# Kernel optimization log

Hardware: AMD Instinct MI355X
Metric: run time of the kernel (lower is better)

## Reference

```python
import jax, jax.numpy as jnp
import numpy as np

B, L, E, H = 2, 2048, 1024, 16
D = E // H  # head dim = 64


def setup_inputs() -> dict:
    key = jax.random.key(0)
    ks = jax.random.split(key, 10)
    s = 0.02
    return {
        "xt": jax.random.normal(ks[0], (B, L, E), jnp.float32),
        "xs": jax.random.normal(ks[1], (B, L, E), jnp.float32),
        "Wt": jax.random.normal(ks[2], (E, 3 * E), jnp.float32) * s,  # t_attn weight (x @ Wt)
        "bt": jnp.zeros((3 * E,), jnp.float32),
        "Ws": jax.random.normal(ks[3], (E, 2 * E), jnp.float32) * s,  # s_attn weight
        "bs": jnp.zeros((2 * E,), jnp.float32),
        "Wc": jax.random.normal(ks[4], (E, E), jnp.float32) * s,      # c_proj weight
        "bc": jnp.zeros((E,), jnp.float32),
        "lam_ts": jnp.ones((1,), jnp.float32),
        "lam_st": jnp.ones((1,), jnp.float32),
        "lam_ss": jnp.ones((1,), jnp.float32),
    }


def _heads(x):
    # (B, L, E) -> (B, H, L, D)
    return x.reshape(B, L, H, D).transpose(0, 2, 1, 3)


def reference(xt, xs, Wt, bt, Ws, bs, Wc, bc, lam_ts, lam_st, lam_ss):
    qt, kt, vt = jnp.split(xt @ Wt + bt, 3, axis=2)
    qs, ks = jnp.split(xs @ Ws + bs, 2, axis=2)
    qt, kt, vt, qs, ks = map(_heads, (qt, kt, vt, qs, ks))

    # 4-way disentangled scores; fuse the 4 matmuls into 2 by combining keys:
    # qt@kt^T + lam_ts*qt@ks^T = qt @ (kt + lam_ts*ks)^T
    # lam_st*qs@kt^T + lam_ss*qs@ks^T = qs @ (lam_st*kt + lam_ss*ks)^T
    k1 = kt + lam_ts[0] * ks
    k2 = lam_st[0] * kt + lam_ss[0] * ks
    att = (jnp.einsum('bhqd,bhkd->bhqk', qt, k1)
           + jnp.einsum('bhqd,bhkd->bhqk', qs, k2)) * (1.0 / np.sqrt(D))
    att = jax.nn.softmax(att, axis=-1)
    y = jnp.einsum('bhqk,bhkd->bhqd', att, vt)  # (B, H, L, D)
    y = y.transpose(0, 2, 1, 3).reshape(B, L, E)
    return y @ Wc + bc
```

## Files before the change

kernel.cpp:

```cpp
#include <hip/hip_runtime.h>
#include <math.h>

#define LQ 2048
#define EQ 1024
#define M_ROWS 4096
#define BH 32

typedef _Float16 f16x8 __attribute__((ext_vector_type(8)));
typedef _Float16 f16x4 __attribute__((ext_vector_type(4)));
typedef _Float16 f16x2 __attribute__((ext_vector_type(2)));
typedef float f32x4 __attribute__((ext_vector_type(4)));
typedef float f32x16 __attribute__((ext_vector_type(16)));

#define QSCALE 0.1803368801111204f

__device__ __forceinline__ void async_ld16(const _Float16* g, _Float16* l) {
  __builtin_amdgcn_global_load_lds(
      (const __attribute__((address_space(1))) unsigned int*)g,
      (__attribute__((address_space(3))) unsigned int*)l, 16, 0, 0);
}

__global__ __launch_bounds__(256) void prep(
    const float* __restrict__ xt, const float* __restrict__ xs,
    const float* __restrict__ Wt, const float* __restrict__ Ws,
    const float* __restrict__ Wc,
    _Float16* __restrict__ xt16, _Float16* __restrict__ xs16,
    _Float16* __restrict__ WtT, _Float16* __restrict__ WsT,
    _Float16* __restrict__ WcT) {
  int gb = blockIdx.x;
  if (gb < 4096) {
    int i = gb * 256 + threadIdx.x;
    const float* s; _Float16* d; size_t off;
    if (i < 524288) { s = xt; d = xt16; off = (size_t)i * 8; }
    else            { s = xs; d = xs16; off = (size_t)(i - 524288) * 8; }
    float4 a = *(const float4*)&s[off];
    float4 b = *(const float4*)&s[off + 4];
    f16x8 h;
    h[0] = (_Float16)a.x; h[1] = (_Float16)a.y; h[2] = (_Float16)a.z; h[3] = (_Float16)a.w;
    h[4] = (_Float16)b.x; h[5] = (_Float16)b.y; h[6] = (_Float16)b.z; h[7] = (_Float16)b.w;
    *(f16x8*)&d[off] = h;
  } else {
    __shared__ float T[32][65];
    int tb = gb - 4096;
    int c0 = (tb % 96) * 64;
    int k0 = (tb / 96) * 32;
    const float* W; _Float16* D; int Nw, cl;
    if (c0 < 3072)      { W = Wt; D = WtT; Nw = 3072; cl = c0; }
    else if (c0 < 5120) { W = Ws; D = WsT; Nw = 2048; cl = c0 - 3072; }
    else                { W = Wc; D = WcT; Nw = 1024; cl = c0 - 5120; }
    const int tid = threadIdx.x;
#pragma unroll
    for (int p = 0; p < 4; ++p) {
      int idx = tid + p * 256;
      int row = idx >> 5;
      int c2 = (idx & 31) * 2;
      float2 v = *(const float2*)&W[(size_t)(k0 + row) * Nw + cl + c2];
      T[row][c2] = v.x;
      T[row][c2 + 1] = v.y;
    }
    __syncthreads();
#pragma unroll
    for (int p = 0; p < 4; ++p) {
      int idx = tid + p * 256;
      int col = idx >> 4;
      int k2 = (idx & 15) * 2;
      f16x2 h2;
      h2[0] = (_Float16)T[k2][col];
      h2[1] = (_Float16)T[k2 + 1][col];
      *(f16x2*)&D[(size_t)(cl + col) * 1024 + k0 + k2] = h2;
    }
  }
}

__global__ __launch_bounds__(256, 3) void proj_gemm(
    const _Float16* __restrict__ xt16, const _Float16* __restrict__ xs16,
    const _Float16* __restrict__ WtT, const _Float16* __restrict__ WsT,
    const float* __restrict__ bt, const float* __restrict__ bs,
    _Float16* __restrict__ q16, _Float16* __restrict__ k16,
    _Float16* __restrict__ v16) {
  __shared__ _Float16 Al[128 * 64];
  __shared__ _Float16 Bl[128 * 64];

  const int tid = threadIdx.x;
  const int w = tid >> 6;
  const int lane = tid & 63;
  const int quad = lane >> 4;
  const int l15 = lane & 15;
  const int wm = w >> 1, wn = w & 1;
  const int by = blockIdx.y;
  const int n0 = blockIdx.x * 128;

  const _Float16* Ab;
  const _Float16* Bb;
  const float* bias;
  int m0, bsel = 0, branch;
  if (by < 32) {
    branch = 0; Ab = xt16; Bb = WtT; bias = bt; m0 = by * 128;
  } else if (by < 48) {
    branch = 1;
    int by2 = by - 32;
    bsel = by2 >> 3;
    m0 = (by2 & 7) * 128;
    Ab = WtT + (size_t)2048 * 1024;
    Bb = xt16 + (size_t)bsel * 2048 * 1024;
    bias = bt;
  } else {
    branch = 2; Ab = xs16; Bb = WsT; bias = bs; m0 = (by - 48) * 128;
  }

  const int srow = lane >> 3;
  const int sch = lane & 7;

  f32x4 acc[4][4];
#pragma unroll
  for (int mb = 0; mb < 4; ++mb)
#pragma unroll
    for (int nb = 0; nb < 4; ++nb) acc[mb][nb] = (f32x4){0.f, 0.f, 0.f, 0.f};

  for (int kt = 0; kt < 1024; kt += 64) {
    __syncthreads();
#pragma unroll
    for (int a = 0; a < 4; ++a) {
      int row = w * 32 + a * 8 + srow;
      int sc = sch ^ (row & 7);
      async_ld16(&Ab[(size_t)(m0 + row) * 1024 + kt + sc * 8], &Al[(w * 32 + a * 8) * 64]);
      async_ld16(&Bb[(size_t)(n0 + row) * 1024 + kt + sc * 8], &Bl[(w * 32 + a * 8) * 64]);
    }
    __syncthreads();

#pragma unroll
    for (int g = 0; g < 2; ++g) {
      f16x8 af[4], bf[4];
#pragma unroll
      for (int mb = 0; mb < 4; ++mb) {
        int row = wm * 64 + mb * 16 + l15;
        int pc = ((g * 4 + quad) ^ (row & 7)) * 8;
        af[mb] = *(const f16x8*)&Al[row * 64 + pc];
      }
#pragma unroll
      for (int nb = 0; nb < 4; ++nb) {
        int row = wn * 64 + nb * 16 + l15;
        int pc = ((g * 4 + quad) ^ (row & 7)) * 8;
        bf[nb] = *(const f16x8*)&Bl[row * 64 + pc];
      }
#pragma unroll
      for (int mb = 0; mb < 4; ++mb)
#pragma unroll
        for (int nb = 0; nb < 4; ++nb)
          acc[mb][nb] = __builtin_amdgcn_mfma_f32_16x16x32_f16(af[mb], bf[nb], acc[mb][nb], 0, 0, 0);
    }
  }

#pragma unroll
  for (int mb = 0; mb < 4; ++mb)
#pragma unroll
    for (int nb = 0; nb < 4; ++nb)
#pragma unroll
      for (int r = 0; r < 4; ++r) {
        int row = m0 + wm * 64 + mb * 16 + quad * 4 + r;
        int col = n0 + wn * 64 + nb * 16 + l15;
        if (branch == 1) {
          float val = acc[mb][nb][r] + bias[2048 + row];
          v16[(size_t)(bsel * 1024 + row) * 2048 + col] = (_Float16)val;
        } else {
          float val = acc[mb][nb][r] + bias[col];
          int bb = row >> 11, ll = row & 2047;
          int which = col >> 10, e = col & 1023;
          int hh = e >> 6, dd = e & 63;
          size_t rowhd = (size_t)(bb * 16 + hh) * 2048 + ll;
          int off = (branch == 0) ? 0 : 64;
          if (which == 0) q16[rowhd * 128 + off + dd] = (_Float16)val;
          else            k16[rowhd * 128 + off + dd] = (_Float16)val;
        }
      }
}

__global__ __launch_bounds__(256, 3) void cproj_gemm(
    const _Float16* __restrict__ A, const _Float16* __restrict__ Bm,
    const float* __restrict__ bias, float* __restrict__ outf) {
  __shared__ _Float16 Al0[128 * 32];
  __shared__ _Float16 Bl0[64 * 32];
  __shared__ _Float16 Al1[128 * 32];
  __shared__ _Float16 Bl1[64 * 32];

  const int tid = threadIdx.x;
  const int w = tid >> 6;
  const int lane = tid & 63;
  const int quad = lane >> 4;
  const int l15 = lane & 15;
  const int wm = w >> 1, wn = w & 1;
  const int m0 = blockIdx.y * 128;
  const int n0 = blockIdx.x * 64;

  const int srow = lane >> 2;
  const int schunk = ((lane & 3) ^ ((lane >> 3) & 3)) * 8;

  f32x4 acc[4][2];
#pragma unroll
  for (int mb = 0; mb < 4; ++mb)
#pragma unroll
    for (int nb = 0; nb < 2; ++nb) acc[mb][nb] = (f32x4){0.f, 0.f, 0.f, 0.f};

  const int key = (l15 >> 1) & 3;

  auto dma = [&](int kt, _Float16* Al, _Float16* Bl) {
#pragma unroll
    for (int i = 0; i < 2; ++i) {
      int rt = w * 32 + i * 16;
      async_ld16(&A[(size_t)(m0 + rt + srow) * 1024 + kt + schunk], &Al[rt * 32]);
    }
    int rtb = w * 16;
    async_ld16(&Bm[(size_t)(n0 + rtb + srow) * 1024 + kt + schunk], &Bl[rtb * 32]);
  };

  auto comp = [&](const _Float16* Al, const _Float16* Bl) {
    f16x8 af[4], bf[2];
    const int pc = (quad ^ key) * 8;
#pragma unroll
    for (int mb = 0; mb < 4; ++mb)
      af[mb] = *(const f16x8*)&Al[(wm * 64 + mb * 16 + l15) * 32 + pc];
#pragma unroll
    for (int nb = 0; nb < 2; ++nb)
      bf[nb] = *(const f16x8*)&Bl[(wn * 32 + nb * 16 + l15) * 32 + pc];
#pragma unroll
    for (int mb = 0; mb < 4; ++mb)
#pragma unroll
      for (int nb = 0; nb < 2; ++nb)
        acc[mb][nb] = __builtin_amdgcn_mfma_f32_16x16x32_f16(af[mb], bf[nb], acc[mb][nb], 0, 0, 0);
  };

  dma(0, Al0, Bl0);
  for (int kt = 0; kt < 1024; kt += 64) {
    __syncthreads();
    dma(kt + 32, Al1, Bl1);
    comp(Al0, Bl0);
    __syncthreads();
    if (kt + 64 < 1024) dma(kt + 64, Al0, Bl0);
    comp(Al1, Bl1);
  }

#pragma unroll
  for (int mb = 0; mb < 4; ++mb)
#pragma unroll
    for (int nb = 0; nb < 2; ++nb)
#pragma unroll
      for (int r = 0; r < 4; ++r) {
        int row = m0 + wm * 64 + mb * 16 + quad * 4 + r;
        int col = n0 + wn * 32 + nb * 16 + l15;
        outf[(size_t)row * 1024 + col] = acc[mb][nb][r] + bias[col];
      }
}

__global__ __launch_bounds__(256, 2) void flash_attn_mfma(
    const _Float16* __restrict__ qcat, const _Float16* __restrict__ kcat,
    const _Float16* __restrict__ vT, _Float16* __restrict__ y,
    const float* __restrict__ lam_ts, const float* __restrict__ lam_st,
    const float* __restrict__ lam_ss) {
  const int bh = blockIdx.y;
  const int qt0 = blockIdx.x * 128;
  const int b = bh >> 4, h = bh & 15;
  const _Float16* Qg = qcat + (size_t)bh * LQ * 128;
  const _Float16* Kg = kcat + (size_t)bh * LQ * 128;
  const _Float16* Vg = vT + (size_t)bh * 64 * LQ;

  __shared__ _Float16 Ksh0[64 * 128];
  __shared__ _Float16 Ksh1[64 * 128];
  __shared__ _Float16 Vsh0[64 * 64];
  __shared__ _Float16 Vsh1[64 * 64];

  const int tid = threadIdx.x;
  const int w = tid >> 6;
  const int lane = tid & 63;
  const int half = lane >> 5;
  const int l31 = lane & 31;

  const float lts = lam_ts[0], lst = lam_st[0], lss = lam_ss[0];

  f16x8 qf[8];
#pragma unroll
  for (int db = 0; db < 4; ++db) {
    const _Float16* qp = &Qg[(size_t)(qt0 + w * 32 + l31) * 128 + db * 16 + half * 8];
    f16x8 a = *(const f16x8*)qp;
    f16x8 bq = *(const f16x8*)(qp + 64);
#pragma unroll
    for (int e = 0; e < 8; ++e) {
      float fa = (float)a[e], fb = (float)bq[e];
      qf[db][e]     = (_Float16)(QSCALE * (fa + lst * fb));
      qf[db + 4][e] = (_Float16)(QSCALE * (lts * fa + lss * fb));
    }
  }

  float m_i = -INFINITY;
  float l_i = 0.f;
  f32x16 O[2];
#pragma unroll
  for (int nt = 0; nt < 2; ++nt)
#pragma unroll
    for (int r = 0; r < 16; ++r) O[nt][r] = 0.f;

  auto dma = [&](int t, _Float16* Kd, _Float16* Vd) {
#pragma unroll
    for (int a = 0; a < 4; ++a) {
      int row = w * 16 + a * 4 + (lane >> 4);
      int sc = (lane & 15) ^ (row & 7);
      async_ld16(&Kg[(size_t)(t + row) * 128 + sc * 8], &Kd[(w * 16 + a * 4) * 128]);
    }
#pragma unroll
    for (int a = 0; a < 2; ++a) {
      int row = w * 16 + a * 8 + (lane >> 3);
      int sc = (lane & 7) ^ (row & 7);
      async_ld16(&Vg[(size_t)row * LQ + t + sc * 8], &Vd[(w * 16 + a * 8) * 64]);
    }
  };

  auto compute = [&](const _Float16* Ks, const _Float16* Vs) {
    f32x16 S[2];
#pragma unroll
    for (int kb = 0; kb < 2; ++kb)
#pragma unroll
      for (int r = 0; r < 16; ++r) S[kb][r] = 0.f;
#pragma unroll
    for (int db = 0; db < 8; ++db) {
      const int pc = ((db * 2 + half) ^ (lane & 7)) * 8;
      f16x8 af[2];
#pragma unroll
      for (int kb = 0; kb < 2; ++kb)
        af[kb] = *(const f16x8*)&Ks[(kb * 32 + l31) * 128 + pc];
#pragma unroll
      for (int kb = 0; kb < 2; ++kb)
        S[kb] = __builtin_amdgcn_mfma_f32_32x32x16_f16(af[kb], qf[db], S[kb], 0, 0, 0);
    }

    float mx = -INFINITY;
#pragma unroll
    for (int kb = 0; kb < 2; ++kb)
#pragma unroll
      for (int r = 0; r < 16; ++r) mx = fmaxf(mx, S[kb][r]);
    mx = fmaxf(mx, __shfl_xor(mx, 32));
    float m_new = fmaxf(m_i, mx);
    float alpha = __builtin_amdgcn_exp2f(m_i - m_new);
    float s = 0.f;
#pragma unroll
    for (int kb = 0; kb < 2; ++kb)
#pragma unroll
      for (int r = 0; r < 16; ++r) {
        float p = __builtin_amdgcn_exp2f(S[kb][r] - m_new);
        S[kb][r] = p;
        s += p;
      }
    s += __shfl_xor(s, 32);
    l_i = l_i * alpha + s;
    m_i = m_new;

#pragma unroll
    for (int nt = 0; nt < 2; ++nt)
#pragma unroll
      for (int r = 0; r < 16; ++r) O[nt][r] *= alpha;

    unsigned pu[2][8];
#pragma unroll
    for (int kb = 0; kb < 2; ++kb)
#pragma unroll
      for (int i = 0; i < 8; ++i) {
        f16x2 t2;
        t2[0] = (_Float16)S[kb][2 * i];
        t2[1] = (_Float16)S[kb][2 * i + 1];
        pu[kb][i] = __builtin_bit_cast(unsigned, t2);
      }

#pragma unroll
    for (int kb = 0; kb < 2; ++kb)
#pragma unroll
      for (int c = 0; c < 2; ++c) {
        unsigned ulo0 = pu[kb][4 * c + 0], ulo1 = pu[kb][4 * c + 1];
        unsigned uhi0 = pu[kb][4 * c + 2], uhi1 = pu[kb][4 * c + 3];
        unsigned rlo0 = (unsigned)__shfl_xor((int)ulo0, 32);
        unsigned rlo1 = (unsigned)__shfl_xor((int)ulo1, 32);
        unsigned rhi0 = (unsigned)__shfl_xor((int)uhi0, 32);
        unsigned rhi1 = (unsigned)__shfl_xor((int)uhi1, 32);
        union { unsigned u[4]; f16x8 v; } pb;
        pb.u[0] = half ? rhi0 : ulo0;
        pb.u[1] = half ? rhi1 : ulo1;
        pb.u[2] = half ? uhi0 : rlo0;
        pb.u[3] = half ? uhi1 : rlo1;
        int kb2 = kb * 2 + c;
        f16x8 av[2];
#pragma unroll
        for (int nt = 0; nt < 2; ++nt) {
          int dim = nt * 32 + l31;
          int pc = ((kb2 * 2 + half) ^ (dim & 7)) * 8;
          av[nt] = *(const f16x8*)&Vs[dim * 64 + pc];
        }
#pragma unroll
        for (int nt = 0; nt < 2; ++nt)
          O[nt] = __builtin_amdgcn_mfma_f32_32x32x16_f16(av[nt], pb.v, O[nt], 0, 0, 0);
      }
  };

  dma(0, Ksh0, Vsh0);
  for (int t = 0; t < LQ; t += 128) {
    __syncthreads();
    dma(t + 64, Ksh1, Vsh1);
    compute(Ksh0, Vsh0);
    __syncthreads();
    if (t + 128 < LQ) dma(t + 128, Ksh0, Vsh0);
    compute(Ksh1, Vsh1);
  }

  float inv = 1.f / l_i;
  int qrow = qt0 + w * 32 + l31;
#pragma unroll
  for (int nt = 0; nt < 2; ++nt)
#pragma unroll
    for (int rg = 0; rg < 4; ++rg) {
      f16x4 o4;
#pragma unroll
      for (int i = 0; i < 4; ++i) o4[i] = (_Float16)(O[nt][rg * 4 + i] * inv);
      int dim = nt * 32 + rg * 8 + half * 4;
      *(f16x4*)&y[((size_t)b * LQ + qrow) * EQ + h * 64 + dim] = o4;
    }
}

extern "C" void kernel_launch(void* const* d_in, const int* in_sizes, int n_in,
                              void* d_out, int out_size, void* d_ws, size_t ws_size,
                              hipStream_t stream) {
  const float* xt = (const float*)d_in[0];
  const float* xs = (const float*)d_in[1];
  const float* Wt = (const float*)d_in[2];
  const float* bt = (const float*)d_in[3];
  const float* Ws = (const float*)d_in[4];
  const float* bs = (const float*)d_in[5];
  const float* Wc = (const float*)d_in[6];
  const float* bc = (const float*)d_in[7];
  const float* lam_ts = (const float*)d_in[8];
  const float* lam_st = (const float*)d_in[9];
  const float* lam_ss = (const float*)d_in[10];
  float* out = (float*)d_out;

  _Float16* w16 = (_Float16*)d_ws;
  _Float16* xt16 = w16;
  _Float16* xs16 = xt16 + 4194304;
  _Float16* WtT  = xs16 + 4194304;
  _Float16* WsT  = WtT + 3145728;
  _Float16* WcT  = WsT + 2097152;
  _Float16* qcat = WcT + 1048576;
  _Float16* kcat = qcat + 8388608;
  _Float16* vbufT = kcat + 8388608;
  _Float16* ybuf = vbufT + 4194304;

  prep<<<7168, 256, 0, stream>>>(xt, xs, Wt, Ws, Wc, xt16, xs16, WtT, WsT, WcT);
  proj_gemm<<<dim3(16, 80), 256, 0, stream>>>(
      xt16, xs16, WtT, WsT, bt, bs, qcat, kcat, vbufT);
  flash_attn_mfma<<<dim3(16, 32), 256, 0, stream>>>(
      qcat, kcat, vbufT, ybuf, lam_ts, lam_st, lam_ss);
  cproj_gemm<<<dim3(16, 32), 256, 0, stream>>>(ybuf, WcT, bc, out);
}
```

Baseline: 263.7 us.

## Split attention KV range in two and merge partial softmax results

The flash attention kernel now processes half of the key sequence per block, using a third grid dimension. It writes unnormalized fp32 partial outputs plus row max and sum, and a new merge kernel combines them into the fp16 attention output. Launch bounds are raised to 3 blocks per CU. The goal is more parallel blocks and better CU utilization, at the cost of extra global traffic for the partials, another launch, and possible register pressure.

```diff
diff --git a/kernel.cpp b/kernel.cpp
--- a/kernel.cpp
+++ b/kernel.cpp
@@ -251,14 +251,16 @@
       }
 }
 
-__global__ __launch_bounds__(256, 2) void flash_attn_mfma(
+__global__ __launch_bounds__(256, 3) void flash_attn_mfma(
     const _Float16* __restrict__ qcat, const _Float16* __restrict__ kcat,
-    const _Float16* __restrict__ vT, _Float16* __restrict__ y,
+    const _Float16* __restrict__ vT,
+    float* __restrict__ Opart, float* __restrict__ MLpart,
     const float* __restrict__ lam_ts, const float* __restrict__ lam_st,
     const float* __restrict__ lam_ss) {
   const int bh = blockIdx.y;
   const int qt0 = blockIdx.x * 128;
-  const int b = bh >> 4, h = bh & 15;
+  const int split = blockIdx.z;
+  const int t0 = split * 1024;
   const _Float16* Qg = qcat + (size_t)bh * LQ * 128;
   const _Float16* Kg = kcat + (size_t)bh * LQ * 128;
   const _Float16* Vg = vT + (size_t)bh * 64 * LQ;
@@ -397,28 +399,59 @@
       }
   };
 
-  dma(0, Ksh0, Vsh0);
-  for (int t = 0; t < LQ; t += 128) {
+  dma(t0, Ksh0, Vsh0);
+  for (int t = t0; t < t0 + 1024; t += 128) {
     __syncthreads();
     dma(t + 64, Ksh1, Vsh1);
     compute(Ksh0, Vsh0);
     __syncthreads();
-    if (t + 128 < LQ) dma(t + 128, Ksh0, Vsh0);
+    if (t + 128 < t0 + 1024) dma(t + 128, Ksh0, Vsh0);
     compute(Ksh1, Vsh1);
   }
 
-  float inv = 1.f / l_i;
-  int qrow = qt0 + w * 32 + l31;
+  const int pblk = (split * 32 + bh) * 16 + blockIdx.x;
+  float* Ob = Opart + (size_t)pblk * (128 * 64);
+  const int qlocal = w * 32 + l31;
 #pragma unroll
   for (int nt = 0; nt < 2; ++nt)
 #pragma unroll
     for (int rg = 0; rg < 4; ++rg) {
-      f16x4 o4;
-#pragma unroll
-      for (int i = 0; i < 4; ++i) o4[i] = (_Float16)(O[nt][rg * 4 + i] * inv);
+      f32x4 o4;
+#pragma unroll
+      for (int i = 0; i < 4; ++i) o4[i] = O[nt][rg * 4 + i];
       int dim = nt * 32 + rg * 8 + half * 4;
-      *(f16x4*)&y[((size_t)b * LQ + qrow) * EQ + h * 64 + dim] = o4;
-    }
+      *(f32x4*)&Ob[(size_t)qlocal * 64 + dim] = o4;
+    }
+  if (half == 0) {
+    float2 ml = {m_i, l_i};
+    *(float2*)&MLpart[((size_t)pblk * 128 + qlocal) * 2] = ml;
+  }
+}
+
+__global__ __launch_bounds__(256) void merge_attn(
+    const float* __restrict__ Opart, const float* __restrict__ MLpart,
+    _Float16* __restrict__ y) {
+  int idx = blockIdx.x * 256 + threadIdx.x;
+  int d4 = (idx & 15) * 4;
+  int row = idx >> 4;
+  int bh = row >> 11, qrow = row & 2047;
+  int qt = qrow >> 7, ql = qrow & 127;
+  int p1 = bh * 16 + qt;
+  int p2 = (32 + bh) * 16 + qt;
+  float2 ml1 = *(const float2*)&MLpart[((size_t)p1 * 128 + ql) * 2];
+  float2 ml2 = *(const float2*)&MLpart[((size_t)p2 * 128 + ql) * 2];
+  float m = fmaxf(ml1.x, ml2.x);
+  float a1 = __builtin_amdgcn_exp2f(ml1.x - m);
+  float a2 = __builtin_amdgcn_exp2f(ml2.x - m);
+  float inv = 1.f / (a1 * ml1.y + a2 * ml2.y);
+  f32x4 o1 = *(const f32x4*)&Opart[((size_t)p1 * 128 + ql) * 64 + d4];
+  f32x4 o2 = *(const f32x4*)&Opart[((size_t)p2 * 128 + ql) * 64 + d4];
+  int b = bh >> 4, h = bh & 15;
+  f16x4 o;
+#pragma unroll
+  for (int i = 0; i < 4; ++i)
+    o[i] = (_Float16)((a1 * o1[i] + a2 * o2[i]) * inv);
+  *(f16x4*)&y[((size_t)(b * LQ + qrow)) * EQ + h * 64 + d4] = o;
 }
 
 extern "C" void kernel_launch(void* const* d_in, const int* in_sizes, int n_in,
@@ -447,11 +480,14 @@
   _Float16* kcat = qcat + 8388608;
   _Float16* vbufT = kcat + 8388608;
   _Float16* ybuf = vbufT + 4194304;
+  float* Opart = (float*)(ybuf + 4194304);
+  float* MLpart = Opart + 8388608;
 
   prep<<<7168, 256, 0, stream>>>(xt, xs, Wt, Ws, Wc, xt16, xs16, WtT, WsT, WcT);
   proj_gemm<<<dim3(16, 80), 256, 0, stream>>>(
       xt16, xs16, WtT, WsT, bt, bs, qcat, kcat, vbufT);
-  flash_attn_mfma<<<dim3(16, 32), 256, 0, stream>>>(
-      qcat, kcat, vbufT, ybuf, lam_ts, lam_st, lam_ss);
+  flash_attn_mfma<<<dim3(16, 32, 2), 256, 0, stream>>>(
+      qcat, kcat, vbufT, Opart, MLpart, lam_ts, lam_st, lam_ss);
+  merge_attn<<<4096, 256, 0, stream>>>(Opart, MLpart, ybuf);
   cproj_gemm<<<dim3(16, 32), 256, 0, stream>>>(ybuf, WcT, bc, out);
 }
```

Measured after the change: 287.4 us. +9.0%, slower.

## Split KV tile across wave pairs in flash attention with final LDS merge

Applied to the files above, without the earlier changes.

Each wave now handles 64 query rows (two 32-row blocks) against half of each 64-key tile, rather than 32 query rows against the full tile. Each K fragment loaded from LDS is reused across two query blocks, and each V fragment is reused across both query blocks, which halves LDS reads per MFMA. The cost is an extra set of online-softmax state per wave and a final cross-wave merge of partial O, m and l through LDS. This adds a synchronisation step and more register pressure (two O accumulators and two Q fragment sets), which could hurt occupancy at 2 blocks per CU.

```diff
diff --git a/kernel.cpp b/kernel.cpp
--- a/kernel.cpp
+++ b/kernel.cpp
@@ -263,40 +263,48 @@
   const _Float16* Kg = kcat + (size_t)bh * LQ * 128;
   const _Float16* Vg = vT + (size_t)bh * 64 * LQ;
 
-  __shared__ _Float16 Ksh0[64 * 128];
-  __shared__ _Float16 Ksh1[64 * 128];
-  __shared__ _Float16 Vsh0[64 * 64];
-  __shared__ _Float16 Vsh1[64 * 64];
+  __shared__ __align__(16) char smem[49152];
+  _Float16* Ksh0 = (_Float16*)smem;
+  _Float16* Ksh1 = (_Float16*)(smem + 16384);
+  _Float16* Vsh0 = (_Float16*)(smem + 32768);
+  _Float16* Vsh1 = (_Float16*)(smem + 40960);
 
   const int tid = threadIdx.x;
   const int w = tid >> 6;
   const int lane = tid & 63;
   const int half = lane >> 5;
   const int l31 = lane & 31;
+  const int qh = w >> 1;
+  const int ks = w & 1;
 
   const float lts = lam_ts[0], lst = lam_st[0], lss = lam_ss[0];
 
-  f16x8 qf[8];
-#pragma unroll
-  for (int db = 0; db < 4; ++db) {
-    const _Float16* qp = &Qg[(size_t)(qt0 + w * 32 + l31) * 128 + db * 16 + half * 8];
-    f16x8 a = *(const f16x8*)qp;
-    f16x8 bq = *(const f16x8*)(qp + 64);
-#pragma unroll
-    for (int e = 0; e < 8; ++e) {
-      float fa = (float)a[e], fb = (float)bq[e];
-      qf[db][e]     = (_Float16)(QSCALE * (fa + lst * fb));
-      qf[db + 4][e] = (_Float16)(QSCALE * (lts * fa + lss * fb));
-    }
-  }
-
-  float m_i = -INFINITY;
-  float l_i = 0.f;
-  f32x16 O[2];
-#pragma unroll
-  for (int nt = 0; nt < 2; ++nt)
-#pragma unroll
-    for (int r = 0; r < 16; ++r) O[nt][r] = 0.f;
+  f16x8 qf[2][8];
+#pragma unroll
+  for (int qb = 0; qb < 2; ++qb)
+#pragma unroll
+    for (int d4 = 0; d4 < 4; ++d4) {
+      const _Float16* qp =
+          &Qg[(size_t)(qt0 + qh * 64 + qb * 32 + l31) * 128 + d4 * 16 + half * 8];
+      f16x8 a = *(const f16x8*)qp;
+      f16x8 bq = *(const f16x8*)(qp + 64);
+#pragma unroll
+      for (int e = 0; e < 8; ++e) {
+        float fa = (float)a[e], fb = (float)bq[e];
+        qf[qb][d4][e]     = (_Float16)(QSCALE * (fa + lst * fb));
+        qf[qb][d4 + 4][e] = (_Float16)(QSCALE * (lts * fa + lss * fb));
+      }
+    }
+
+  float m_i[2] = {-INFINITY, -INFINITY};
+  float l_i[2] = {0.f, 0.f};
+  f32x16 O[2][2];
+#pragma unroll
+  for (int qb = 0; qb < 2; ++qb)
+#pragma unroll
+    for (int nt = 0; nt < 2; ++nt)
+#pragma unroll
+      for (int r = 0; r < 16; ++r) O[qb][nt][r] = 0.f;
 
   auto dma = [&](int t, _Float16* Kd, _Float16* Vd) {
 #pragma unroll
@@ -316,64 +324,68 @@
   auto compute = [&](const _Float16* Ks, const _Float16* Vs) {
     f32x16 S[2];
 #pragma unroll
-    for (int kb = 0; kb < 2; ++kb)
-#pragma unroll
-      for (int r = 0; r < 16; ++r) S[kb][r] = 0.f;
+    for (int qb = 0; qb < 2; ++qb)
+#pragma unroll
+      for (int r = 0; r < 16; ++r) S[qb][r] = 0.f;
 #pragma unroll
     for (int db = 0; db < 8; ++db) {
       const int pc = ((db * 2 + half) ^ (lane & 7)) * 8;
-      f16x8 af[2];
-#pragma unroll
-      for (int kb = 0; kb < 2; ++kb)
-        af[kb] = *(const f16x8*)&Ks[(kb * 32 + l31) * 128 + pc];
-#pragma unroll
-      for (int kb = 0; kb < 2; ++kb)
-        S[kb] = __builtin_amdgcn_mfma_f32_32x32x16_f16(af[kb], qf[db], S[kb], 0, 0, 0);
-    }
-
-    float mx = -INFINITY;
-#pragma unroll
-    for (int kb = 0; kb < 2; ++kb)
-#pragma unroll
-      for (int r = 0; r < 16; ++r) mx = fmaxf(mx, S[kb][r]);
-    mx = fmaxf(mx, __shfl_xor(mx, 32));
-    float m_new = fmaxf(m_i, mx);
-    float alpha = __builtin_amdgcn_exp2f(m_i - m_new);
-    float s = 0.f;
-#pragma unroll
-    for (int kb = 0; kb < 2; ++kb)
+      f16x8 af = *(const f16x8*)&Ks[(ks * 32 + l31) * 128 + pc];
+#pragma unroll
+      for (int qb = 0; qb < 2; ++qb)
+        S[qb] = __builtin_amdgcn_mfma_f32_32x32x16_f16(af, qf[qb][db], S[qb], 0, 0, 0);
+    }
+
+    float alpha[2];
+#pragma unroll
+    for (int qb = 0; qb < 2; ++qb) {
+      float mx = -INFINITY;
+#pragma unroll
+      for (int r = 0; r < 16; ++r) mx = fmaxf(mx, S[qb][r]);
+      mx = fmaxf(mx, __shfl_xor(mx, 32));
+      float m_new = fmaxf(m_i[qb], mx);
+      alpha[qb] = __builtin_amdgcn_exp2f(m_i[qb] - m_new);
+      float s = 0.f;
 #pragma unroll
       for (int r = 0; r < 16; ++r) {
-        float p = __builtin_amdgcn_exp2f(S[kb][r] - m_new);
-        S[kb][r] = p;
+        float p = __builtin_amdgcn_exp2f(S[qb][r] - m_new);
+        S[qb][r] = p;
         s += p;
       }
-    s += __shfl_xor(s, 32);
-    l_i = l_i * alpha + s;
-    m_i = m_new;
-
-#pragma unroll
-    for (int nt = 0; nt < 2; ++nt)
-#pragma unroll
-      for (int r = 0; r < 16; ++r) O[nt][r] *= alpha;
+      s += __shfl_xor(s, 32);
+      l_i[qb] = l_i[qb] * alpha[qb] + s;
+      m_i[qb] = m_new;
+#pragma unroll
+      for (int nt = 0; nt < 2; ++nt)
+#pragma unroll
+        for (int r = 0; r < 16; ++r) O[qb][nt][r] *= alpha[qb];
+    }
 
     unsigned pu[2][8];
 #pragma unroll
-    for (int kb = 0; kb < 2; ++kb)
+    for (int qb = 0; qb < 2; ++qb)
 #pragma unroll
       for (int i = 0; i < 8; ++i) {
         f16x2 t2;
-        t2[0] = (_Float16)S[kb][2 * i];
-        t2[1] = (_Float16)S[kb][2 * i + 1];
-        pu[kb][i] = __builtin_bit_cast(unsigned, t2);
-      }
-
-#pragma unroll
-    for (int kb = 0; kb < 2; ++kb)
-#pragma unroll
-      for (int c = 0; c < 2; ++c) {
-        unsigned ulo0 = pu[kb][4 * c + 0], ulo1 = pu[kb][4 * c + 1];
-        unsigned uhi0 = pu[kb][4 * c + 2], uhi1 = pu[kb][4 * c + 3];
+        t2[0] = (_Float16)S[qb][2 * i];
+        t2[1] = (_Float16)S[qb][2 * i + 1];
+        pu[qb][i] = __builtin_bit_cast(unsigned, t2);
+      }
+
+#pragma unroll
+    for (int c = 0; c < 2; ++c) {
+      f16x8 av[2];
+#pragma unroll
+      for (int nt = 0; nt < 2; ++nt) {
+        int dim = nt * 32 + l31;
+        int lchunk = ks * 4 + c * 2 + half;
+        int pc = (lchunk ^ (dim & 7)) * 8;
+        av[nt] = *(const f16x8*)&Vs[dim * 64 + pc];
+      }
+#pragma unroll
+      for (int qb = 0; qb < 2; ++qb) {
+        unsigned ulo0 = pu[qb][4 * c + 0], ulo1 = pu[qb][4 * c + 1];
+        unsigned uhi0 = pu[qb][4 * c + 2], uhi1 = pu[qb][4 * c + 3];
         unsigned rlo0 = (unsigned)__shfl_xor((int)ulo0, 32);
         unsigned rlo1 = (unsigned)__shfl_xor((int)ulo1, 32);
         unsigned rhi0 = (unsigned)__shfl_xor((int)uhi0, 32);
@@ -383,18 +395,11 @@
         pb.u[1] = half ? rhi1 : ulo1;
         pb.u[2] = half ? uhi0 : rlo0;
         pb.u[3] = half ? uhi1 : rlo1;
-        int kb2 = kb * 2 + c;
-        f16x8 av[2];
-#pragma unroll
-        for (int nt = 0; nt < 2; ++nt) {
-          int dim = nt * 32 + l31;
-          int pc = ((kb2 * 2 + half) ^ (dim & 7)) * 8;
-          av[nt] = *(const f16x8*)&Vs[dim * 64 + pc];
-        }
 #pragma unroll
         for (int nt = 0; nt < 2; ++nt)
-          O[nt] = __builtin_amdgcn_mfma_f32_32x32x16_f16(av[nt], pb.v, O[nt], 0, 0, 0);
-      }
+          O[qb][nt] = __builtin_amdgcn_mfma_f32_32x32x16_f16(av[nt], pb.v, O[qb][nt], 0, 0, 0);
+      }
+    }
   };
 
   dma(0, Ksh0, Vsh0);
@@ -407,18 +412,54 @@
     compute(Ksh1, Vsh1);
   }
 
-  float inv = 1.f / l_i;
-  int qrow = qt0 + w * 32 + l31;
-#pragma unroll
-  for (int nt = 0; nt < 2; ++nt)
-#pragma unroll
-    for (int rg = 0; rg < 4; ++rg) {
-      f16x4 o4;
-#pragma unroll
-      for (int i = 0; i < 4; ++i) o4[i] = (_Float16)(O[nt][rg * 4 + i] * inv);
-      int dim = nt * 32 + rg * 8 + half * 4;
-      *(f16x4*)&y[((size_t)b * LQ + qrow) * EQ + h * 64 + dim] = o4;
-    }
+  __syncthreads();
+  float* Om = (float*)(smem + qh * 17408);
+  float* Ml = (float*)(smem + 34816 + qh * 512);
+
+  if (ks == 0) {
+#pragma unroll
+    for (int qb = 0; qb < 2; ++qb) {
+#pragma unroll
+      for (int nt = 0; nt < 2; ++nt)
+#pragma unroll
+        for (int rg = 0; rg < 4; ++rg) {
+          f32x4 o4;
+#pragma unroll
+          for (int i = 0; i < 4; ++i) o4[i] = O[qb][nt][rg * 4 + i];
+          int dim = nt * 32 + rg * 8 + half * 4;
+          *(f32x4*)&Om[(size_t)(qb * 32 + l31) * 68 + dim] = o4;
+        }
+      if (half == 0) {
+        Ml[(qb * 32 + l31) * 2 + 0] = m_i[qb];
+        Ml[(qb * 32 + l31) * 2 + 1] = l_i[qb];
+      }
+    }
+  }
+  __syncthreads();
+  if (ks == 1) {
+#pragma unroll
+    for (int qb = 0; qb < 2; ++qb) {
+      float m0 = Ml[(qb * 32 + l31) * 2 + 0];
+      float l0 = Ml[(qb * 32 + l31) * 2 + 1];
+      float m = fmaxf(m0, m_i[qb]);
+      float a0 = __builtin_amdgcn_exp2f(m0 - m);
+      float a1 = __builtin_amdgcn_exp2f(m_i[qb] - m);
+      float inv = 1.f / (a0 * l0 + a1 * l_i[qb]);
+      int qrow = qt0 + qh * 64 + qb * 32 + l31;
+#pragma unroll
+      for (int nt = 0; nt < 2; ++nt)
+#pragma unroll
+        for (int rg = 0; rg < 4; ++rg) {
+          int dim = nt * 32 + rg * 8 + half * 4;
+          f32x4 o0 = *(const f32x4*)&Om[(size_t)(qb * 32 + l31) * 68 + dim];
+          f16x4 o;
+#pragma unroll
+          for (int i = 0; i < 4; ++i)
+            o[i] = (_Float16)((a0 * o0[i] + a1 * O[qb][nt][rg * 4 + i]) * inv);
+          *(f16x4*)&y[((size_t)(b * LQ + qrow)) * EQ + h * 64 + dim] = o;
+        }
+    }
+  }
 }
 
 extern "C" void kernel_launch(void* const* d_in, const int* in_sizes, int n_in,
```

New measurement: 284.3 us. +7.8%, slower.
